# Kernel tuning notes

Hardware: AMD Instinct MI355X
Metric: run time of the kernel (lower is better)

The kernel has to match this reference:

```python
import jax, jax.numpy as jnp
import numpy as np

N_NODES = 100000
N_EDGES = 1600000
D_IN = 256
D_OUT = 64


def setup_inputs() -> dict:
    key = jax.random.key(0)
    k1, k2, k3, k4, k5 = jax.random.split(key, 5)
    features = jax.random.normal(k1, (N_NODES, D_IN), dtype=jnp.float32)
    # Xavier-uniform style init for the weight
    limit = float(np.sqrt(6.0 / (D_IN + D_OUT)))
    weight = jax.random.uniform(k2, (D_IN, D_OUT), minval=-limit, maxval=limit, dtype=jnp.float32)
    adj_rows = jax.random.randint(k3, (N_EDGES,), 0, N_NODES, dtype=jnp.int64)
    adj_cols = jax.random.randint(k4, (N_EDGES,), 0, N_NODES, dtype=jnp.int64)
    adj_values = jax.random.uniform(k5, (N_EDGES,), dtype=jnp.float32)
    return {"features": features, "weight": weight, "adj_rows": adj_rows,
            "adj_cols": adj_cols, "adj_values": adj_values}


def reference(features, weight, adj_rows, adj_cols, adj_values):
    # support = features @ W  -> [N, D_OUT]
    support = jnp.matmul(features, weight)
    # spmm: out[r] = sum_e (v_e * support[c_e]) for edges (r, c, v)
    msgs = adj_values[:, None] * support[adj_cols]  # [E, D_OUT]
    output = jax.ops.segment_sum(msgs, adj_rows, num_segments=features.shape[0])
    # active=True -> ReLU fused on the aggregation output
    return jax.nn.relu(output)
```

## Files before the change

### kernel.cpp

```cpp
#include <hip/hip_runtime.h>

#define N_NODES 100000
#define N_EDGES 1600000
#define D_IN    256
#define D_OUT   64

#define BROWS 256
#define NBUCK ((N_NODES + BROWS - 1) / BROWS)
#define CAP   8192
#define EB    8192
#define NB1   ((N_EDGES + EB - 1) / EB)
#define MAXB  8192

typedef __attribute__((ext_vector_type(8))) short short8_t;
typedef __attribute__((ext_vector_type(4))) float f32x4;

static __device__ __forceinline__ unsigned short f2bf(float f) {
    unsigned u = __builtin_bit_cast(unsigned, f);
    unsigned r = u + 0x7FFFu + ((u >> 16) & 1u);
    return (unsigned short)(r >> 16);
}
static __device__ __forceinline__ float bf2f(unsigned short h) {
    return __builtin_bit_cast(float, (unsigned)h << 16);
}

__global__ __launch_bounds__(256) void gemm_kernel(const float* __restrict__ feat,
                                                   const float* __restrict__ W,
                                                   unsigned short* __restrict__ support,
                                                   int* __restrict__ gcursor) {
    __shared__ unsigned short Wf[2048 * 8];
    const int tid = threadIdx.x;

    if (blockIdx.x == 0) {
        for (int i = tid; i < NBUCK; i += 256) gcursor[i] = i * CAP;
    }

    #pragma unroll
    for (int i = 0; i < 8; ++i) {
        const int slot = i * 256 + tid;
        const int s  = slot >> 8;
        const int nt = (slot >> 6) & 3;
        const int l  = slot & 63;
        const int kbase = s * 32 + ((l >> 4) * 8);
        const int col   = nt * 16 + (l & 15);
        unsigned short tmp[8];
        #pragma unroll
        for (int e = 0; e < 8; ++e)
            tmp[e] = f2bf(W[(size_t)(kbase + e) * D_OUT + col]);
        *(short8_t*)&Wf[slot * 8] = *(short8_t*)tmp;
    }
    __syncthreads();

    const int lane = tid & 63;
    const int wave = tid >> 6;
    const int row0 = blockIdx.x * 64 + wave * 16;
    if (row0 >= N_NODES) return;

    const float* arow = feat + (size_t)(row0 + (lane & 15)) * D_IN + ((lane >> 4) * 8);

    f32x4 acc[4];
    #pragma unroll
    for (int nt = 0; nt < 4; ++nt) acc[nt] = (f32x4){0.f, 0.f, 0.f, 0.f};

    #pragma unroll
    for (int s = 0; s < 8; ++s) {
        const float4 a0 = *(const float4*)(arow + s * 32);
        const float4 a1 = *(const float4*)(arow + s * 32 + 4);
        unsigned short af[8];
        af[0] = f2bf(a0.x); af[1] = f2bf(a0.y); af[2] = f2bf(a0.z); af[3] = f2bf(a0.w);
        af[4] = f2bf(a1.x); af[5] = f2bf(a1.y); af[6] = f2bf(a1.z); af[7] = f2bf(a1.w);
        const short8_t av = *(short8_t*)af;
        #pragma unroll
        for (int nt = 0; nt < 4; ++nt) {
            const short8_t bv = *(short8_t*)&Wf[((s * 4 + nt) * 64 + lane) * 8];
            acc[nt] = __builtin_amdgcn_mfma_f32_16x16x32_bf16(av, bv, acc[nt], 0, 0, 0);
        }
    }

    #pragma unroll
    for (int nt = 0; nt < 4; ++nt) {
        #pragma unroll
        for (int reg = 0; reg < 4; ++reg) {
            const int row = row0 + (lane >> 4) * 4 + reg;
            const int col = nt * 16 + (lane & 15);
            support[(size_t)row * D_OUT + col] = f2bf(acc[nt][reg]);
        }
    }
}

__global__ __launch_bounds__(1024) void bscatter_kernel(const int*   __restrict__ rows,
                                                        const int*   __restrict__ cols,
                                                        const float* __restrict__ vals,
                                                        int*  __restrict__ gcursor,
                                                        int2* __restrict__ pack) {
    __shared__ int lrows[EB];
    __shared__ int h[NBUCK];
    __shared__ int base[NBUCK];
    const int tid = threadIdx.x;
    for (int i = tid; i < NBUCK; i += 1024) h[i] = 0;
    __syncthreads();

    const int e0 = blockIdx.x * EB;
    for (int i = tid; i < EB; i += 1024) {
        const int e = e0 + i;
        const int r = (e < N_EDGES) ? rows[e] : -1;
        lrows[i] = r;
        if (r >= 0) atomicAdd(&h[r >> 8], 1);
    }
    __syncthreads();

    for (int b = tid; b < NBUCK; b += 1024) {
        const int c = h[b];
        base[b] = c ? atomicAdd(&gcursor[b], c) : 0;
        h[b] = 0;
    }
    __syncthreads();

    for (int i = tid; i < EB; i += 1024) {
        const int r = lrows[i];
        if (r < 0) continue;
        const int b = r >> 8;
        const int pos = base[b] + atomicAdd(&h[b], 1);
        if (pos < (b + 1) * CAP) {
            const int e = e0 + i;
            pack[pos] = make_int2(((r & 255) << 17) | cols[e], __float_as_int(vals[e]));
        }
    }
}

__global__ __launch_bounds__(1024) void breduce_kernel(const int*  __restrict__ gcursor,
                                                       const int2* __restrict__ pack,
                                                       const unsigned short* __restrict__ support,
                                                       float* __restrict__ out) {
    __shared__ int2 ps[MAXB];
    __shared__ int cnt[BROWS];
    __shared__ int ofs[BROWS];
    __shared__ int cur[BROWS];
    __shared__ int scn[BROWS];
    const int b     = blockIdx.x;
    const int tid   = threadIdx.x;
    const int start = b * CAP;
    int n = gcursor[b] - start;
    if (n > MAXB) n = MAXB;
    const int lane  = tid & 63;
    const int wave  = tid >> 6;

    if (tid < BROWS) cnt[tid] = 0;
    __syncthreads();

    for (int i = tid; i < n; i += 1024)
        atomicAdd(&cnt[pack[start + i].x >> 17], 1);
    __syncthreads();

    const int v = (tid < BROWS) ? cnt[tid] : 0;
    if (tid < BROWS) scn[tid] = v;
    __syncthreads();
    #pragma unroll
    for (int off = 1; off < BROWS; off <<= 1) {
        const int t = (tid < BROWS && tid >= off) ? scn[tid - off] : 0;
        __syncthreads();
        if (tid < BROWS) scn[tid] += t;
        __syncthreads();
    }
    if (tid < BROWS) { ofs[tid] = scn[tid] - v; cur[tid] = 0; }
    __syncthreads();

    for (int i = tid; i < n; i += 1024) {
        const int2 p  = pack[start + i];
        const int  rl = p.x >> 17;
        ps[ofs[rl] + atomicAdd(&cur[rl], 1)] = p;
    }
    __syncthreads();

    for (int rl = wave; rl < BROWS; rl += 16) {
        const int row = b * BROWS + rl;
        if (row >= N_NODES) continue;
        const int s0 = ofs[rl];
        const int nr = cnt[rl];
        float a0 = 0.f, a1 = 0.f, a2 = 0.f, a3 = 0.f;
        int k = 0;
        for (; k + 3 < nr; k += 4) {
            const int2 p0 = ps[s0 + k];
            const int2 p1 = ps[s0 + k + 1];
            const int2 p2 = ps[s0 + k + 2];
            const int2 p3 = ps[s0 + k + 3];
            a0 = fmaf(__int_as_float(p0.y), bf2f(support[(size_t)(p0.x & 0x1FFFF) * D_OUT + lane]), a0);
            a1 = fmaf(__int_as_float(p1.y), bf2f(support[(size_t)(p1.x & 0x1FFFF) * D_OUT + lane]), a1);
            a2 = fmaf(__int_as_float(p2.y), bf2f(support[(size_t)(p2.x & 0x1FFFF) * D_OUT + lane]), a2);
            a3 = fmaf(__int_as_float(p3.y), bf2f(support[(size_t)(p3.x & 0x1FFFF) * D_OUT + lane]), a3);
        }
        for (; k < nr; ++k) {
            const int2 p = ps[s0 + k];
            a0 = fmaf(__int_as_float(p.y), bf2f(support[(size_t)(p.x & 0x1FFFF) * D_OUT + lane]), a0);
        }
        out[(size_t)row * D_OUT + lane] = fmaxf((a0 + a1) + (a2 + a3), 0.0f);
    }
}

extern "C" void kernel_launch(void* const* d_in, const int* in_sizes, int n_in,
                              void* d_out, int out_size, void* d_ws, size_t ws_size,
                              hipStream_t stream) {
    const float* feat = (const float*)d_in[0];
    const float* W    = (const float*)d_in[1];
    const int*   rows = (const int*)d_in[2];
    const int*   cols = (const int*)d_in[3];
    const float* vals = (const float*)d_in[4];
    float*       out  = (float*)d_out;

    unsigned short* support = (unsigned short*)d_ws;
    int*   gcursor = (int*)(support + 6400000);
    int2*  pack    = (int2*)(gcursor + 392);

    gemm_kernel<<<(N_NODES + 63) / 64, 256, 0, stream>>>(feat, W, support, gcursor);

    bscatter_kernel<<<NB1, 1024, 0, stream>>>(rows, cols, vals, gcursor, pack);

    breduce_kernel<<<NBUCK, 1024, 0, stream>>>(gcursor, pack, support, out);
}
```

Baseline: 89.02 us.

## Use packed bf16 convert in GEMM and half-wave paired gather in SpMM reduce

In the GEMM, per-element software bf16 rounding is replaced with the hardware v_cvt_pk_bf16_f32 instruction, converting two floats per instruction. In the reduce kernel, each wave now splits into two halves that handle alternate edges. Each lane loads two bf16 columns as one 32-bit word, and the halves are combined with a cross-half shuffle before a float2 store. This is meant to widen the per-lane gather loads and cut the number of dependent loop iterations per row, at the cost of a shuffle and half the lanes idle on the final store.

```diff
diff --git a/kernel.cpp b/kernel.cpp
--- a/kernel.cpp
+++ b/kernel.cpp
@@ -22,6 +22,11 @@
 }
 static __device__ __forceinline__ float bf2f(unsigned short h) {
     return __builtin_bit_cast(float, (unsigned)h << 16);
+}
+static __device__ __forceinline__ unsigned cvt_pk_bf16(float lo, float hi) {
+    unsigned r;
+    asm("v_cvt_pk_bf16_f32 %0, %1, %2" : "=v"(r) : "v"(lo), "v"(hi));
+    return r;
 }
 
 __global__ __launch_bounds__(256) void gemm_kernel(const float* __restrict__ feat,
@@ -66,10 +71,12 @@
     for (int s = 0; s < 8; ++s) {
         const float4 a0 = *(const float4*)(arow + s * 32);
         const float4 a1 = *(const float4*)(arow + s * 32 + 4);
-        unsigned short af[8];
-        af[0] = f2bf(a0.x); af[1] = f2bf(a0.y); af[2] = f2bf(a0.z); af[3] = f2bf(a0.w);
-        af[4] = f2bf(a1.x); af[5] = f2bf(a1.y); af[6] = f2bf(a1.z); af[7] = f2bf(a1.w);
-        const short8_t av = *(short8_t*)af;
+        unsigned u[4];
+        u[0] = cvt_pk_bf16(a0.x, a0.y);
+        u[1] = cvt_pk_bf16(a0.z, a0.w);
+        u[2] = cvt_pk_bf16(a1.x, a1.y);
+        u[3] = cvt_pk_bf16(a1.z, a1.w);
+        const short8_t av = *(short8_t*)u;
         #pragma unroll
         for (int nt = 0; nt < 4; ++nt) {
             const short8_t bv = *(short8_t*)&Wf[((s * 4 + nt) * 64 + lane) * 8];
@@ -144,6 +151,8 @@
     if (n > MAXB) n = MAXB;
     const int lane  = tid & 63;
     const int wave  = tid >> 6;
+    const int half  = lane >> 5;
+    const int cl    = lane & 31;
 
     if (tid < BROWS) cnt[tid] = 0;
     __syncthreads();
@@ -177,23 +186,55 @@
         if (row >= N_NODES) continue;
         const int s0 = ofs[rl];
         const int nr = cnt[rl];
-        float a0 = 0.f, a1 = 0.f, a2 = 0.f, a3 = 0.f;
+        float ax0 = 0.f, ay0 = 0.f, ax1 = 0.f, ay1 = 0.f;
+        float ax2 = 0.f, ay2 = 0.f, ax3 = 0.f, ay3 = 0.f;
         int k = 0;
-        for (; k + 3 < nr; k += 4) {
-            const int2 p0 = ps[s0 + k];
-            const int2 p1 = ps[s0 + k + 1];
-            const int2 p2 = ps[s0 + k + 2];
-            const int2 p3 = ps[s0 + k + 3];
-            a0 = fmaf(__int_as_float(p0.y), bf2f(support[(size_t)(p0.x & 0x1FFFF) * D_OUT + lane]), a0);
-            a1 = fmaf(__int_as_float(p1.y), bf2f(support[(size_t)(p1.x & 0x1FFFF) * D_OUT + lane]), a1);
-            a2 = fmaf(__int_as_float(p2.y), bf2f(support[(size_t)(p2.x & 0x1FFFF) * D_OUT + lane]), a2);
-            a3 = fmaf(__int_as_float(p3.y), bf2f(support[(size_t)(p3.x & 0x1FFFF) * D_OUT + lane]), a3);
-        }
-        for (; k < nr; ++k) {
+        for (; k + 7 < nr; k += 8) {
+            const int2 p0 = ps[s0 + k     + half];
+            const int2 p1 = ps[s0 + k + 2 + half];
+            const int2 p2 = ps[s0 + k + 4 + half];
+            const int2 p3 = ps[s0 + k + 6 + half];
+            const unsigned q0 = *(const unsigned*)&support[(size_t)(p0.x & 0x1FFFF) * D_OUT + 2 * cl];
+            const unsigned q1 = *(const unsigned*)&support[(size_t)(p1.x & 0x1FFFF) * D_OUT + 2 * cl];
+            const unsigned q2 = *(const unsigned*)&support[(size_t)(p2.x & 0x1FFFF) * D_OUT + 2 * cl];
+            const unsigned q3 = *(const unsigned*)&support[(size_t)(p3.x & 0x1FFFF) * D_OUT + 2 * cl];
+            const float v0 = __int_as_float(p0.y);
+            const float v1 = __int_as_float(p1.y);
+            const float v2 = __int_as_float(p2.y);
+            const float v3 = __int_as_float(p3.y);
+            ax0 = fmaf(v0, bf2f((unsigned short)(q0 & 0xFFFF)), ax0);
+            ay0 = fmaf(v0, bf2f((unsigned short)(q0 >> 16)),    ay0);
+            ax1 = fmaf(v1, bf2f((unsigned short)(q1 & 0xFFFF)), ax1);
+            ay1 = fmaf(v1, bf2f((unsigned short)(q1 >> 16)),    ay1);
+            ax2 = fmaf(v2, bf2f((unsigned short)(q2 & 0xFFFF)), ax2);
+            ay2 = fmaf(v2, bf2f((unsigned short)(q2 >> 16)),    ay2);
+            ax3 = fmaf(v3, bf2f((unsigned short)(q3 & 0xFFFF)), ax3);
+            ay3 = fmaf(v3, bf2f((unsigned short)(q3 >> 16)),    ay3);
+        }
+        for (; k + 1 < nr; k += 2) {
+            const int2 p = ps[s0 + k + half];
+            const unsigned q = *(const unsigned*)&support[(size_t)(p.x & 0x1FFFF) * D_OUT + 2 * cl];
+            const float vv = __int_as_float(p.y);
+            ax0 = fmaf(vv, bf2f((unsigned short)(q & 0xFFFF)), ax0);
+            ay0 = fmaf(vv, bf2f((unsigned short)(q >> 16)),    ay0);
+        }
+        if (k < nr && half == 0) {
             const int2 p = ps[s0 + k];
-            a0 = fmaf(__int_as_float(p.y), bf2f(support[(size_t)(p.x & 0x1FFFF) * D_OUT + lane]), a0);
-        }
-        out[(size_t)row * D_OUT + lane] = fmaxf((a0 + a1) + (a2 + a3), 0.0f);
+            const unsigned q = *(const unsigned*)&support[(size_t)(p.x & 0x1FFFF) * D_OUT + 2 * cl];
+            const float vv = __int_as_float(p.y);
+            ax0 = fmaf(vv, bf2f((unsigned short)(q & 0xFFFF)), ax0);
+            ay0 = fmaf(vv, bf2f((unsigned short)(q >> 16)),    ay0);
+        }
+        float sx = (ax0 + ax1) + (ax2 + ax3);
+        float sy = (ay0 + ay1) + (ay2 + ay3);
+        sx += __shfl_xor(sx, 32, 64);
+        sy += __shfl_xor(sy, 32, 64);
+        if (half == 0) {
+            float2 o;
+            o.x = fmaxf(sx, 0.f);
+            o.y = fmaxf(sy, 0.f);
+            *(float2*)&out[(size_t)row * D_OUT + 2 * cl] = o;
+        }
     }
 }
 
```

Result: faster. 85.88 us (-3.5%).

## Slice support into column passes and gather 8 edges per wave in reduce

Applied to the files above, without the earlier changes.

The GEMM now writes support as four column slices of 16 bf16 values each (32 bytes per row), and uses packed bf16 conversion instructions. The reduce kernel loops over the four slices, and each wave handles 8 edges at once with 8 lanes per edge, each lane loading a u32. Partial sums are combined with cross-lane shuffles. This aims to shrink the gather working set per pass so it fits in cache and to raise memory-level parallelism, at the cost of re-reading the packed edges four times and adding shuffle reductions.

```diff
diff --git a/kernel.cpp b/kernel.cpp
--- a/kernel.cpp
+++ b/kernel.cpp
@@ -11,6 +11,8 @@
 #define EB    8192
 #define NB1   ((N_EDGES + EB - 1) / EB)
 #define MAXB  8192
+#define NPASS 4
+#define SLICE_U32 800000
 
 typedef __attribute__((ext_vector_type(8))) short short8_t;
 typedef __attribute__((ext_vector_type(4))) float f32x4;
@@ -22,6 +24,11 @@
 }
 static __device__ __forceinline__ float bf2f(unsigned short h) {
     return __builtin_bit_cast(float, (unsigned)h << 16);
+}
+static __device__ __forceinline__ unsigned cvt_pk_bf16(float lo, float hi) {
+    unsigned r;
+    asm("v_cvt_pk_bf16_f32 %0, %1, %2" : "=v"(r) : "v"(lo), "v"(hi));
+    return r;
 }
 
 __global__ __launch_bounds__(256) void gemm_kernel(const float* __restrict__ feat,
@@ -66,10 +73,12 @@
     for (int s = 0; s < 8; ++s) {
         const float4 a0 = *(const float4*)(arow + s * 32);
         const float4 a1 = *(const float4*)(arow + s * 32 + 4);
-        unsigned short af[8];
-        af[0] = f2bf(a0.x); af[1] = f2bf(a0.y); af[2] = f2bf(a0.z); af[3] = f2bf(a0.w);
-        af[4] = f2bf(a1.x); af[5] = f2bf(a1.y); af[6] = f2bf(a1.z); af[7] = f2bf(a1.w);
-        const short8_t av = *(short8_t*)af;
+        unsigned u[4];
+        u[0] = cvt_pk_bf16(a0.x, a0.y);
+        u[1] = cvt_pk_bf16(a0.z, a0.w);
+        u[2] = cvt_pk_bf16(a1.x, a1.y);
+        u[3] = cvt_pk_bf16(a1.z, a1.w);
+        const short8_t av = *(short8_t*)u;
         #pragma unroll
         for (int nt = 0; nt < 4; ++nt) {
             const short8_t bv = *(short8_t*)&Wf[((s * 4 + nt) * 64 + lane) * 8];
@@ -82,8 +91,8 @@
         #pragma unroll
         for (int reg = 0; reg < 4; ++reg) {
             const int row = row0 + (lane >> 4) * 4 + reg;
-            const int col = nt * 16 + (lane & 15);
-            support[(size_t)row * D_OUT + col] = f2bf(acc[nt][reg]);
+            support[(size_t)nt * (SLICE_U32 * 2) + (size_t)row * 16 + (lane & 15)]
+                = f2bf(acc[nt][reg]);
         }
     }
 }
@@ -144,6 +153,8 @@
     if (n > MAXB) n = MAXB;
     const int lane  = tid & 63;
     const int wave  = tid >> 6;
+    const int eslot = lane >> 3;
+    const int cp    = lane & 7;
 
     if (tid < BROWS) cnt[tid] = 0;
     __syncthreads();
@@ -172,28 +183,42 @@
     }
     __syncthreads();
 
-    for (int rl = wave; rl < BROWS; rl += 16) {
-        const int row = b * BROWS + rl;
-        if (row >= N_NODES) continue;
-        const int s0 = ofs[rl];
-        const int nr = cnt[rl];
-        float a0 = 0.f, a1 = 0.f, a2 = 0.f, a3 = 0.f;
-        int k = 0;
-        for (; k + 3 < nr; k += 4) {
-            const int2 p0 = ps[s0 + k];
-            const int2 p1 = ps[s0 + k + 1];
-            const int2 p2 = ps[s0 + k + 2];
-            const int2 p3 = ps[s0 + k + 3];
-            a0 = fmaf(__int_as_float(p0.y), bf2f(support[(size_t)(p0.x & 0x1FFFF) * D_OUT + lane]), a0);
-            a1 = fmaf(__int_as_float(p1.y), bf2f(support[(size_t)(p1.x & 0x1FFFF) * D_OUT + lane]), a1);
-            a2 = fmaf(__int_as_float(p2.y), bf2f(support[(size_t)(p2.x & 0x1FFFF) * D_OUT + lane]), a2);
-            a3 = fmaf(__int_as_float(p3.y), bf2f(support[(size_t)(p3.x & 0x1FFFF) * D_OUT + lane]), a3);
-        }
-        for (; k < nr; ++k) {
-            const int2 p = ps[s0 + k];
-            a0 = fmaf(__int_as_float(p.y), bf2f(support[(size_t)(p.x & 0x1FFFF) * D_OUT + lane]), a0);
-        }
-        out[(size_t)row * D_OUT + lane] = fmaxf((a0 + a1) + (a2 + a3), 0.0f);
+    for (int p = 0; p < NPASS; ++p) {
+        const unsigned* slice = (const unsigned*)support + (size_t)p * SLICE_U32;
+        for (int rl = wave; rl < BROWS; rl += 16) {
+            const int row = b * BROWS + rl;
+            if (row >= N_NODES) continue;
+            const int s0 = ofs[rl];
+            const int nr = cnt[rl];
+            float ax0 = 0.f, ay0 = 0.f, ax1 = 0.f, ay1 = 0.f;
+            for (int k = 0; k < nr; k += 16) {
+                const int  iA = k + eslot;
+                const int  iB = k + 8 + eslot;
+                const bool vA = iA < nr;
+                const bool vB = iB < nr;
+                const int2 pA = ps[s0 + (vA ? iA : 0)];
+                const int2 pB = ps[s0 + (vB ? iB : 0)];
+                const float fA = vA ? __int_as_float(pA.y) : 0.f;
+                const float fB = vB ? __int_as_float(pB.y) : 0.f;
+                const unsigned qA = slice[(size_t)(pA.x & 0x1FFFF) * 8 + cp];
+                const unsigned qB = slice[(size_t)(pB.x & 0x1FFFF) * 8 + cp];
+                ax0 = fmaf(fA, bf2f((unsigned short)(qA & 0xFFFF)), ax0);
+                ay0 = fmaf(fA, bf2f((unsigned short)(qA >> 16)),    ay0);
+                ax1 = fmaf(fB, bf2f((unsigned short)(qB & 0xFFFF)), ax1);
+                ay1 = fmaf(fB, bf2f((unsigned short)(qB >> 16)),    ay1);
+            }
+            float sx = ax0 + ax1;
+            float sy = ay0 + ay1;
+            sx += __shfl_xor(sx, 8, 64);   sy += __shfl_xor(sy, 8, 64);
+            sx += __shfl_xor(sx, 16, 64);  sy += __shfl_xor(sy, 16, 64);
+            sx += __shfl_xor(sx, 32, 64);  sy += __shfl_xor(sy, 32, 64);
+            if (eslot == 0) {
+                float2 o;
+                o.x = fmaxf(sx, 0.f);
+                o.y = fmaxf(sy, 0.f);
+                *(float2*)&out[(size_t)row * D_OUT + p * 16 + 2 * cp] = o;
+            }
+        }
     }
 }
 
```

After: 125.8 us. 41.3% more time.
